# Kernel optimization log

Measured on AMD Instinct MI355X. Metric: run time of the kernel, lower is better.

The kernel has to match this reference:

```python
import jax, jax.numpy as jnp
import numpy as np
import math

D_MODEL = 1024
N_HEADS = 16
HEAD_DIM = D_MODEL // N_HEADS  # 64
R = HEAD_DIM // 2              # 32
ROPE_BASE = 10000.0
B, T = 4, 2048


def setup_inputs() -> dict:
    key = jax.random.key(0)
    k1, k2, k3, k4, k5 = jax.random.split(key, 5)
    x = jax.random.normal(k1, (B, T, D_MODEL), dtype=jnp.float32)
    Wqkv = jax.random.normal(k2, (3 * D_MODEL, D_MODEL), dtype=jnp.float32) * (1.0 / math.sqrt(D_MODEL))
    Wout = jax.random.normal(k3, (D_MODEL, D_MODEL), dtype=jnp.float32) * (1.0 / math.sqrt(D_MODEL))
    alpha = jax.random.normal(k4, (N_HEADS, R), dtype=jnp.float32) * 0.01
    beta = jax.random.normal(k5, (N_HEADS, R), dtype=jnp.float32) * 0.01
    return {"x": x, "Wqkv": Wqkv, "Wout": Wout, "alpha": alpha, "beta": beta}


def _fourier_bias(alpha, beta, t):
    # omega[r] = base^{-2r/head_dim}, same geometric spacing as RoPE
    omega = ROPE_BASE ** (-2.0 * jnp.arange(R, dtype=jnp.float32) / HEAD_DIM)
    # bias depends only on displacement i-j in [-(t-1), t-1]: compute once per
    # displacement, then gather into the (t, t) matrix (same math as full T x T).
    disp = jnp.arange(-(t - 1), t, dtype=jnp.float32)            # (2t-1,)
    angles = omega[:, None] * disp[None, :]                       # (R, 2t-1)
    vec = jnp.einsum('hr,rk->hk', alpha, jnp.cos(angles)) \
        + jnp.einsum('hr,rk->hk', beta, jnp.sin(angles))          # (H, 2t-1)
    i = jnp.arange(t)
    idx = i[:, None] - i[None, :] + (t - 1)                       # (t, t), delta[i,j]=i-j
    return vec[:, idx]                                            # (H, t, t)


def reference(x, Wqkv, Wout, alpha, beta):
    b, t, d = x.shape
    qkv = x @ Wqkv.T                                              # (B, T, 3D)
    q, k, v = jnp.split(qkv, 3, axis=-1)
    def heads(a):
        return a.reshape(b, t, N_HEADS, HEAD_DIM).transpose(0, 2, 1, 3)  # (B,H,T,dh)
    q, k, v = heads(q), heads(k), heads(v)
    scale = 1.0 / math.sqrt(HEAD_DIM)
    logits = jnp.einsum('bhqd,bhkd->bhqk', q, k) * scale          # (B,H,T,T)
    logits = logits + _fourier_bias(alpha, beta, t)[None]
    causal = jnp.tril(jnp.ones((t, t), dtype=bool))
    logits = jnp.where(causal[None, None], logits, -jnp.inf)
    attn = jax.nn.softmax(logits, axis=-1)
    out = jnp.einsum('bhqk,bhkd->bhqd', attn, v)                  # (B,H,T,dh)
    out = out.transpose(0, 2, 1, 3).reshape(b, t, d)
    return out @ Wout.T
```

## Files before the change

kernel.cpp:

```cpp
#include <hip/hip_runtime.h>
#include <cstdint>
#include <cstddef>

typedef _Float16 f16;
typedef f16 f16x8 __attribute__((ext_vector_type(8)));
typedef __fp16 fp16x2 __attribute__((ext_vector_type(2)));
typedef float f32x4 __attribute__((ext_vector_type(4)));
typedef float f32x16 __attribute__((ext_vector_type(16)));
typedef uint32_t u32;


__device__ __forceinline__ void gload16(const void* g, void* l) {
  __builtin_amdgcn_global_load_lds((const __attribute__((address_space(1))) void*)g,
                                   (__attribute__((address_space(3))) void*)l,
                                   16u, 0, 0u);
}

__device__ __forceinline__ u32 pkrtz(float a, float b) {
  union { fp16x2 v; u32 u; } t;
  t.v = __builtin_amdgcn_cvt_pkrtz(a, b);
  return t.u;
}

__device__ __forceinline__ u32 packh2(float a, float b) { return pkrtz(a, b); }

__device__ __forceinline__ float max3f(float a, float b, float c) {
  return fmaxf(fmaxf(a, b), c);
}

__device__ __forceinline__ void pl32swap(u32& a, u32& b) {
  asm volatile("v_permlane32_swap_b32 %0, %1" : "+v"(a), "+v"(b));
}


__global__ __launch_bounds__(256) void cvt_f32_f16(const float* __restrict__ in,
                                                   f16* __restrict__ out, int n) {
  int i = (blockIdx.x * 256 + threadIdx.x) * 8;
  if (i >= n) return;
  float4 a = *(const float4*)(in + i);
  float4 b = *(const float4*)(in + i + 4);
  f16x8 o;
  o[0] = (f16)a.x; o[1] = (f16)a.y; o[2] = (f16)a.z; o[3] = (f16)a.w;
  o[4] = (f16)b.x; o[5] = (f16)b.y; o[6] = (f16)b.z; o[7] = (f16)b.w;
  *(f16x8*)(out + i) = o;
}


__global__ __launch_bounds__(256) void build_tables(const float* __restrict__ alpha,
                                                    const float* __restrict__ beta,
                                                    f16* __restrict__ U,
                                                    f16* __restrict__ Wt) {
  int idx = blockIdx.x * 256 + threadIdx.x;
  int t = idx >> 5, r = idx & 31;
  float w = powf(10000.0f, -(float)r / 32.0f);
  float ang = w * (float)t;
  float c = cosf(ang), s = sinf(ang);
  const float L2E = 1.44269504089f;
  U[t * 64 + 2 * r]     = (f16)(c * L2E);
  U[t * 64 + 2 * r + 1] = (f16)(s * L2E);
  #pragma unroll
  for (int h = 0; h < 16; ++h) {
    float al = alpha[h * 32 + r], be = beta[h * 32 + r];
    Wt[(size_t)(h * 2048 + t) * 64 + 2 * r]     = (f16)(al * c - be * s);
    Wt[(size_t)(h * 2048 + t) * 64 + 2 * r + 1] = (f16)(al * s + be * c);
  }
}


__global__ __launch_bounds__(256) void gemm_qkv(const f16* __restrict__ A,
                                                const f16* __restrict__ B,
                                                f16* __restrict__ Q,
                                                f16* __restrict__ Kh,
                                                f16* __restrict__ Vt) {
  __shared__ __align__(16) char sm[65536];
  const int K = 1024;
  int tid = threadIdx.x;
  int lane = tid & 63, wid = tid >> 6;
  int bid = blockIdx.x;
  int xcd = bid & 7;
  int id = bid >> 3;
  int nl = id / 64;
  int m0 = (id & 63) * 128;
  int n0 = (xcd * 3 + nl) * 128;
  int wm = wid >> 1, wn = wid & 1;
  int c = lane & 15, g = lane >> 4, l7 = lane & 7;

  int srow[4], sce[4], sdst[4];
  #pragma unroll
  for (int i = 0; i < 4; ++i) {
    int p = i * 4096 + tid * 16;
    int q = p ^ (((p >> 7) & 7) << 4);
    srow[i] = q >> 7; sce[i] = (q & 127) >> 1;
    sdst[i] = i * 4096 + wid * 1024;
  }

  f32x4 acc[4][4] = {};

  #pragma unroll
  for (int i = 0; i < 4; ++i) {
    gload16(A + (size_t)(m0 + srow[i]) * K + sce[i], sm + sdst[i]);
    gload16(B + (size_t)(n0 + srow[i]) * K + sce[i], sm + 32768 + sdst[i]);
  }

  for (int kt = 0; kt < 16; ++kt) {
    int cur = kt & 1;
    char* As = sm + cur * 16384;
    char* Bs = sm + 32768 + cur * 16384;

    if (kt < 15) {
      char* Ad = sm + (cur ^ 1) * 16384;
      char* Bd = sm + 32768 + (cur ^ 1) * 16384;
      #pragma unroll
      for (int i = 0; i < 4; ++i) {
        gload16(A + (size_t)(m0 + srow[i]) * K + (kt + 1) * 64 + sce[i], Ad + sdst[i]);
        gload16(B + (size_t)(n0 + srow[i]) * K + (kt + 1) * 64 + sce[i], Bd + sdst[i]);
      }
      asm volatile("s_waitcnt vmcnt(8)" ::: "memory");
    } else {
      asm volatile("s_waitcnt vmcnt(0)" ::: "memory");
    }
    __builtin_amdgcn_s_barrier();

    __builtin_amdgcn_s_setprio(1);
    #pragma unroll
    for (int kk = 0; kk < 2; ++kk) {
      int co = (kk * 64 + g * 16) ^ (l7 << 4);
      f16x8 af[4], bf[4];
      #pragma unroll
      for (int fr = 0; fr < 4; ++fr)
        af[fr] = *(const f16x8*)(As + (wm * 64 + fr * 16 + c) * 128 + co);
      #pragma unroll
      for (int fn = 0; fn < 4; ++fn)
        bf[fn] = *(const f16x8*)(Bs + (wn * 64 + fn * 16 + c) * 128 + co);
      #pragma unroll
      for (int fr = 0; fr < 4; ++fr)
        #pragma unroll
        for (int fn = 0; fn < 4; ++fn)
          acc[fr][fn] = __builtin_amdgcn_mfma_f32_16x16x32_f16(af[fr], bf[fn], acc[fr][fn], 0, 0, 0);
    }
    __builtin_amdgcn_s_setprio(0);
    __builtin_amdgcn_s_barrier();
  }

  int which = n0 >> 10;
  #pragma unroll
  for (int fr = 0; fr < 4; ++fr) {
    int m = m0 + wm * 64 + fr * 16 + g * 4;
    int b = m >> 11, t = m & 2047;
    #pragma unroll
    for (int fn = 0; fn < 4; ++fn) {
      int n = n0 + wn * 64 + fn * 16 + c;
      int nf = n & 1023, hh = nf >> 6, d = nf & 63;
      if (which == 0) {
        #pragma unroll
        for (int r = 0; r < 4; ++r)
          Q[(size_t)((b * 16 + hh) * 2048 + (t + r)) * 64 + d] = (f16)(acc[fr][fn][r] * 0.180336880111f);
      } else if (which == 1) {
        #pragma unroll
        for (int r = 0; r < 4; ++r)
          Kh[(size_t)((b * 16 + hh) * 2048 + (t + r)) * 64 + d] = (f16)acc[fr][fn][r];
      } else {
        uint2 pk;
        pk.x = packh2(acc[fr][fn][0], acc[fr][fn][1]);
        pk.y = packh2(acc[fr][fn][2], acc[fr][fn][3]);
        *(uint2*)(Vt + (size_t)((b * 16 + hh) * 64 + d) * 2048 + t) = pk;
      }
    }
  }
}


__global__ __launch_bounds__(256) void gemm_out(const f16* __restrict__ A,
                                                const f16* __restrict__ B,
                                                float* __restrict__ Cout) {
  __shared__ __align__(16) char sm[65536];
  const int K = 1024;
  int tid = threadIdx.x;
  int lane = tid & 63, wid = tid >> 6;
  int bid = blockIdx.x;
  int xcd = bid & 7;
  int id = bid >> 3;
  int m0 = id * 128;
  int n0 = xcd * 128;
  int wm = wid >> 1, wn = wid & 1;
  int c = lane & 15, g = lane >> 4, l7 = lane & 7;

  int srow[4], sce[4], sdst[4];
  #pragma unroll
  for (int i = 0; i < 4; ++i) {
    int p = i * 4096 + tid * 16;
    int q = p ^ (((p >> 7) & 7) << 4);
    srow[i] = q >> 7; sce[i] = (q & 127) >> 1;
    sdst[i] = i * 4096 + wid * 1024;
  }

  f32x4 acc[4][4] = {};

  #pragma unroll
  for (int i = 0; i < 4; ++i) {
    gload16(A + (size_t)(m0 + srow[i]) * K + sce[i], sm + sdst[i]);
    gload16(B + (size_t)(n0 + srow[i]) * K + sce[i], sm + 32768 + sdst[i]);
  }

  for (int kt = 0; kt < 16; ++kt) {
    int cur = kt & 1;
    char* As = sm + cur * 16384;
    char* Bs = sm + 32768 + cur * 16384;

    if (kt < 15) {
      char* Ad = sm + (cur ^ 1) * 16384;
      char* Bd = sm + 32768 + (cur ^ 1) * 16384;
      #pragma unroll
      for (int i = 0; i < 4; ++i) {
        gload16(A + (size_t)(m0 + srow[i]) * K + (kt + 1) * 64 + sce[i], Ad + sdst[i]);
        gload16(B + (size_t)(n0 + srow[i]) * K + (kt + 1) * 64 + sce[i], Bd + sdst[i]);
      }
      asm volatile("s_waitcnt vmcnt(8)" ::: "memory");
    } else {
      asm volatile("s_waitcnt vmcnt(0)" ::: "memory");
    }
    __builtin_amdgcn_s_barrier();

    __builtin_amdgcn_s_setprio(1);
    #pragma unroll
    for (int kk = 0; kk < 2; ++kk) {
      int co = (kk * 64 + g * 16) ^ (l7 << 4);
      f16x8 af[4], bf[4];
      #pragma unroll
      for (int fr = 0; fr < 4; ++fr)
        af[fr] = *(const f16x8*)(As + (wm * 64 + fr * 16 + c) * 128 + co);
      #pragma unroll
      for (int fn = 0; fn < 4; ++fn)
        bf[fn] = *(const f16x8*)(Bs + (wn * 64 + fn * 16 + c) * 128 + co);
      #pragma unroll
      for (int fr = 0; fr < 4; ++fr)
        #pragma unroll
        for (int fn = 0; fn < 4; ++fn)
          acc[fr][fn] = __builtin_amdgcn_mfma_f32_16x16x32_f16(af[fr], bf[fn], acc[fr][fn], 0, 0, 0);
    }
    __builtin_amdgcn_s_setprio(0);
    __builtin_amdgcn_s_barrier();
  }

  #pragma unroll
  for (int fr = 0; fr < 4; ++fr) {
    int m = m0 + wm * 64 + fr * 16 + g * 4;
    #pragma unroll
    for (int fn = 0; fn < 4; ++fn) {
      int n = n0 + wn * 64 + fn * 16 + c;
      #pragma unroll
      for (int r = 0; r < 4; ++r)
        Cout[(size_t)(m + r) * 1024 + n] = acc[fr][fn][r];
    }
  }
}


__global__ __launch_bounds__(512, 2) void attn(const f16* __restrict__ Q,
                                               const f16* __restrict__ Kh,
                                               const f16* __restrict__ Vt,
                                               const f16* __restrict__ U,
                                               const f16* __restrict__ Wt,
                                               f16* __restrict__ AO) {
  __shared__ __align__(16) char sm[98304];
  int tid = threadIdx.x, lane = tid & 63, wid = tid >> 6;
  int l31 = lane & 31, hi = lane >> 5;
  int o = blockIdx.x;
  int pr = o >> 6;
  int bh = o & 63;
  int h = bh & 15, b = bh >> 4;
  int swz = (lane & 15) << 4;

  const f16* ksrc[4]; int kdst[4];
  #pragma unroll
  for (int i = 0; i < 4; ++i) {
    int p = i * 8192 + tid * 16;
    int row = p >> 8;
    int col = (p & 255) ^ ((row & 15) << 4);
    int ce = col >> 1;
    ksrc[i] = (ce < 64) ? (Kh + (size_t)(bh * 2048 + row) * 64 + ce)
                        : (Wt + (size_t)(h * 2048 + row) * 64 + (ce - 64));
    kdst[i] = i * 8192 + wid * 1024;
  }
  const f16* vsrc[2]; int vdst[2];
  #pragma unroll
  for (int i = 0; i < 2; ++i) {
    int p = i * 8192 + tid * 16;
    int row = p >> 8;
    int col = (p & 255) ^ ((row & 15) << 4);
    int ce = col >> 1;
    vsrc[i] = Vt + (size_t)(bh * 64 + row) * 2048 + ce;
    vdst[i] = i * 8192 + wid * 1024;
  }

  #pragma unroll 1
  for (int pass = 0; pass < 2; ++pass) {
    int qt = pass ? pr : 7 - pr;
    int qrow = qt * 256 + wid * 32 + l31;
    int ktmax = 2 * qt + 1;

    f16x8 qf[8];
    {
      const f16* qp = Q + (size_t)(bh * 2048 + qrow) * 64 + hi * 8;
      const f16* up = U + (size_t)qrow * 64 + hi * 8;
      #pragma unroll
      for (int ks = 0; ks < 4; ++ks) {
        qf[ks]     = *(const f16x8*)(qp + ks * 16);
        qf[4 + ks] = *(const f16x8*)(up + ks * 16);
      }
    }

    float m_i = -1e30f, l_i = 0.0f;
    f32x16 accA = {}, accB = {};

    #pragma unroll
    for (int i = 0; i < 4; ++i) gload16(ksrc[i], sm + kdst[i]);
    #pragma unroll
    for (int i = 0; i < 2; ++i) gload16(vsrc[i], sm + 65536 + vdst[i]);
    __syncthreads();

    for (int kt = 0; kt <= ktmax; ++kt) {
      int cur = kt & 1;
      char* Ks = sm + cur * 32768;
      char* Vs = sm + 65536 + cur * 16384;

      if (kt < ktmax) {
        char* kb = sm + (cur ^ 1) * 32768;
        char* vb = sm + 65536 + (cur ^ 1) * 16384;
        #pragma unroll
        for (int i = 0; i < 4; ++i) gload16(ksrc[i] + (size_t)(kt + 1) * 8192, kb + kdst[i]);
        #pragma unroll
        for (int i = 0; i < 2; ++i) gload16(vsrc[i] + (size_t)(kt + 1) * 128, vb + vdst[i]);
      }

      f32x16 st0 = {}, st1 = {}, st2 = {}, st3 = {};
      __builtin_amdgcn_s_setprio(1);
      #pragma unroll
      for (int ks = 0; ks < 8; ++ks) {
        int co = (ks * 32 + hi * 16) ^ swz;
        f16x8 k0 = *(const f16x8*)(Ks + l31 * 256 + co);
        f16x8 k1 = *(const f16x8*)(Ks + (32 + l31) * 256 + co);
        f16x8 k2 = *(const f16x8*)(Ks + (64 + l31) * 256 + co);
        f16x8 k3 = *(const f16x8*)(Ks + (96 + l31) * 256 + co);
        st0 = __builtin_amdgcn_mfma_f32_32x32x16_f16(k0, qf[ks], st0, 0, 0, 0);
        st1 = __builtin_amdgcn_mfma_f32_32x32x16_f16(k1, qf[ks], st1, 0, 0, 0);
        st2 = __builtin_amdgcn_mfma_f32_32x32x16_f16(k2, qf[ks], st2, 0, 0, 0);
        st3 = __builtin_amdgcn_mfma_f32_32x32x16_f16(k3, qf[ks], st3, 0, 0, 0);
      }
      __builtin_amdgcn_s_setprio(0);

      int kv0 = kt * 128;
      if (kv0 + 127 > qt * 256 + wid * 32) {
        #pragma unroll
        for (int r = 0; r < 16; ++r) {
          int kvl = kv0 + (r & 3) + 8 * (r >> 2) + 4 * hi;
          if (kvl > qrow) st0[r] = -1e30f;
          if (kvl + 32 > qrow) st1[r] = -1e30f;
          if (kvl + 64 > qrow) st2[r] = -1e30f;
          if (kvl + 96 > qrow) st3[r] = -1e30f;
        }
      }

      float pm = fmaxf(fmaxf(st0[0], st1[0]), fmaxf(st2[0], st3[0]));
      #pragma unroll
      for (int r = 1; r < 16; ++r) {
        pm = max3f(pm, st0[r], st1[r]);
        pm = max3f(pm, st2[r], st3[r]);
      }
      pm = fmaxf(pm, __shfl_xor(pm, 32, 64));
      if (!__all(pm <= m_i + 8.0f)) {
        float mnew = fmaxf(m_i, pm);
        float sc = __builtin_amdgcn_exp2f(m_i - mnew);
        l_i *= sc;
        accA *= sc;
        accB *= sc;
        m_i = mnew;
      }

      float ps = 0.0f;
      u32 pk0[8], pk1[8], pk2[8], pk3[8];
      #pragma unroll
      for (int j = 0; j < 8; ++j) {
        float a0 = __builtin_amdgcn_exp2f(st0[2 * j] - m_i);
        float a1 = __builtin_amdgcn_exp2f(st0[2 * j + 1] - m_i);
        float b0 = __builtin_amdgcn_exp2f(st1[2 * j] - m_i);
        float b1 = __builtin_amdgcn_exp2f(st1[2 * j + 1] - m_i);
        float c0 = __builtin_amdgcn_exp2f(st2[2 * j] - m_i);
        float c1 = __builtin_amdgcn_exp2f(st2[2 * j + 1] - m_i);
        float d0 = __builtin_amdgcn_exp2f(st3[2 * j] - m_i);
        float d1 = __builtin_amdgcn_exp2f(st3[2 * j + 1] - m_i);
        ps += (a0 + a1) + (b0 + b1) + (c0 + c1) + (d0 + d1);
        pk0[j] = pkrtz(a0, a1);
        pk1[j] = pkrtz(b0, b1);
        pk2[j] = pkrtz(c0, c1);
        pk3[j] = pkrtz(d0, d1);
      }
      ps += __shfl_xor(ps, 32, 64);
      l_i += ps;

      pl32swap(pk0[0], pk0[2]); pl32swap(pk0[1], pk0[3]);
      pl32swap(pk0[4], pk0[6]); pl32swap(pk0[5], pk0[7]);
      pl32swap(pk1[0], pk1[2]); pl32swap(pk1[1], pk1[3]);
      pl32swap(pk1[4], pk1[6]); pl32swap(pk1[5], pk1[7]);
      pl32swap(pk2[0], pk2[2]); pl32swap(pk2[1], pk2[3]);
      pl32swap(pk2[4], pk2[6]); pl32swap(pk2[5], pk2[7]);
      pl32swap(pk3[0], pk3[2]); pl32swap(pk3[1], pk3[3]);
      pl32swap(pk3[4], pk3[6]); pl32swap(pk3[5], pk3[7]);

      __builtin_amdgcn_s_setprio(1);
      #pragma unroll
      for (int kb = 0; kb < 8; ++kb) {
        union { u32 w[4]; f16x8 v; } bf;
        const u32* pk = (kb < 2) ? pk0 : (kb < 4) ? pk1 : (kb < 6) ? pk2 : pk3;
        int base = (kb & 1) * 4;
        bf.w[0] = pk[base + 0]; bf.w[1] = pk[base + 1];
        bf.w[2] = pk[base + 2]; bf.w[3] = pk[base + 3];
        int co = (kb * 32 + hi * 16) ^ swz;
        f16x8 v0 = *(const f16x8*)(Vs + l31 * 256 + co);
        f16x8 v1 = *(const f16x8*)(Vs + (32 + l31) * 256 + co);
        accA = __builtin_amdgcn_mfma_f32_32x32x16_f16(v0, bf.v, accA, 0, 0, 0);
        accB = __builtin_amdgcn_mfma_f32_32x32x16_f16(v1, bf.v, accB, 0, 0, 0);
      }
      __builtin_amdgcn_s_setprio(0);
      __syncthreads();
    }

    float inv = __builtin_amdgcn_rcpf(l_i);
    f16* aop = AO + (size_t)(b * 2048 + qrow) * 1024 + h * 64;
    #pragma unroll
    for (int u = 0; u < 4; ++u) {
      uint2 ov;
      ov.x = pkrtz(accA[4 * u] * inv, accA[4 * u + 1] * inv);
      ov.y = pkrtz(accA[4 * u + 2] * inv, accA[4 * u + 3] * inv);
      *(uint2*)(aop + 8 * u + 4 * hi) = ov;
      ov.x = pkrtz(accB[4 * u] * inv, accB[4 * u + 1] * inv);
      ov.y = pkrtz(accB[4 * u + 2] * inv, accB[4 * u + 3] * inv);
      *(uint2*)(aop + 32 + 8 * u + 4 * hi) = ov;
    }
  }
}


extern "C" void kernel_launch(void* const* d_in, const int* in_sizes, int n_in,
                              void* d_out, int out_size, void* d_ws, size_t ws_size,
                              hipStream_t stream) {
  const float* x     = (const float*)d_in[0];
  const float* Wqkv  = (const float*)d_in[1];
  const float* Wout  = (const float*)d_in[2];
  const float* alpha = (const float*)d_in[3];
  const float* beta  = (const float*)d_in[4];

  char* ws = (char*)d_ws;
  f16* Xh    = (f16*)(ws);
  f16* Wqkvh = (f16*)(ws + 16777216);
  f16* Wouth = (f16*)(ws + 23068672);
  f16* Qh    = (f16*)(ws + 25165824);
  f16* Kh    = (f16*)(ws + 41943040);
  f16* Vt    = (f16*)(ws + 58720256);
  f16* U     = (f16*)(ws + 75497472);
  f16* Wt    = (f16*)(ws + 75759616);
  f16* AO    = Xh;

  cvt_f32_f16<<<4096, 256, 0, stream>>>(x, Xh, 8388608);
  cvt_f32_f16<<<1536, 256, 0, stream>>>(Wqkv, Wqkvh, 3145728);
  cvt_f32_f16<<<512, 256, 0, stream>>>(Wout, Wouth, 1048576);
  build_tables<<<256, 256, 0, stream>>>(alpha, beta, U, Wt);
  gemm_qkv<<<1536, 256, 0, stream>>>(Xh, Wqkvh, Qh, Kh, Vt);
  attn<<<256, 512, 0, stream>>>(Qh, Kh, Vt, U, Wt, AO);
  gemm_out<<<512, 256, 0, stream>>>(AO, Wouth, (float*)d_out);
}
```

Measured before the change: 186.4 us.

## Software-pipeline QK^T of next tile with softmax and PV of current tile

Restructures the attention loop so the QK^T MFMAs for the next KV tile are issued before the softmax and PV work of the current tile. K tiles are now prefetched two iterations ahead and V one ahead, with a prologue that loads two K tiles and computes the first scores. The aim is to hide exp/max latency behind matrix-core work, at the cost of another 64 accumulator registers per lane, which may lower occupancy or cause spills.

```diff
diff --git a/kernel.cpp b/kernel.cpp
--- a/kernel.cpp
+++ b/kernel.cpp
@@ -317,23 +317,13 @@
     for (int i = 0; i < 4; ++i) gload16(ksrc[i], sm + kdst[i]);
     #pragma unroll
     for (int i = 0; i < 2; ++i) gload16(vsrc[i], sm + 65536 + vdst[i]);
+    #pragma unroll
+    for (int i = 0; i < 4; ++i) gload16(ksrc[i] + 8192, sm + 32768 + kdst[i]);
     __syncthreads();
 
-    for (int kt = 0; kt <= ktmax; ++kt) {
-      int cur = kt & 1;
-      char* Ks = sm + cur * 32768;
-      char* Vs = sm + 65536 + cur * 16384;
-
-      if (kt < ktmax) {
-        char* kb = sm + (cur ^ 1) * 32768;
-        char* vb = sm + 65536 + (cur ^ 1) * 16384;
-        #pragma unroll
-        for (int i = 0; i < 4; ++i) gload16(ksrc[i] + (size_t)(kt + 1) * 8192, kb + kdst[i]);
-        #pragma unroll
-        for (int i = 0; i < 2; ++i) gload16(vsrc[i] + (size_t)(kt + 1) * 128, vb + vdst[i]);
-      }
-
-      f32x16 st0 = {}, st1 = {}, st2 = {}, st3 = {};
+    f32x16 stC0 = {}, stC1 = {}, stC2 = {}, stC3 = {};
+    {
+      char* Ks = sm;
       __builtin_amdgcn_s_setprio(1);
       #pragma unroll
       for (int ks = 0; ks < 8; ++ks) {
@@ -342,30 +332,64 @@
         f16x8 k1 = *(const f16x8*)(Ks + (32 + l31) * 256 + co);
         f16x8 k2 = *(const f16x8*)(Ks + (64 + l31) * 256 + co);
         f16x8 k3 = *(const f16x8*)(Ks + (96 + l31) * 256 + co);
-        st0 = __builtin_amdgcn_mfma_f32_32x32x16_f16(k0, qf[ks], st0, 0, 0, 0);
-        st1 = __builtin_amdgcn_mfma_f32_32x32x16_f16(k1, qf[ks], st1, 0, 0, 0);
-        st2 = __builtin_amdgcn_mfma_f32_32x32x16_f16(k2, qf[ks], st2, 0, 0, 0);
-        st3 = __builtin_amdgcn_mfma_f32_32x32x16_f16(k3, qf[ks], st3, 0, 0, 0);
+        stC0 = __builtin_amdgcn_mfma_f32_32x32x16_f16(k0, qf[ks], stC0, 0, 0, 0);
+        stC1 = __builtin_amdgcn_mfma_f32_32x32x16_f16(k1, qf[ks], stC1, 0, 0, 0);
+        stC2 = __builtin_amdgcn_mfma_f32_32x32x16_f16(k2, qf[ks], stC2, 0, 0, 0);
+        stC3 = __builtin_amdgcn_mfma_f32_32x32x16_f16(k3, qf[ks], stC3, 0, 0, 0);
       }
       __builtin_amdgcn_s_setprio(0);
+    }
+
+    for (int kt = 0; kt <= ktmax; ++kt) {
+      char* Vs = sm + 65536 + (kt & 1) * 16384;
+
+      if (kt + 1 <= ktmax) {
+        char* vb = sm + 65536 + ((kt + 1) & 1) * 16384;
+        #pragma unroll
+        for (int i = 0; i < 2; ++i) gload16(vsrc[i] + (size_t)(kt + 1) * 128, vb + vdst[i]);
+      }
+      if (kt + 2 <= ktmax) {
+        char* kb = sm + (kt & 1) * 32768;
+        #pragma unroll
+        for (int i = 0; i < 4; ++i) gload16(ksrc[i] + (size_t)(kt + 2) * 8192, kb + kdst[i]);
+      }
+
+      f32x16 stN0 = {}, stN1 = {}, stN2 = {}, stN3 = {};
+      if (kt < ktmax) {
+        char* Ks = sm + ((kt + 1) & 1) * 32768;
+        __builtin_amdgcn_s_setprio(1);
+        #pragma unroll
+        for (int ks = 0; ks < 8; ++ks) {
+          int co = (ks * 32 + hi * 16) ^ swz;
+          f16x8 k0 = *(const f16x8*)(Ks + l31 * 256 + co);
+          f16x8 k1 = *(const f16x8*)(Ks + (32 + l31) * 256 + co);
+          f16x8 k2 = *(const f16x8*)(Ks + (64 + l31) * 256 + co);
+          f16x8 k3 = *(const f16x8*)(Ks + (96 + l31) * 256 + co);
+          stN0 = __builtin_amdgcn_mfma_f32_32x32x16_f16(k0, qf[ks], stN0, 0, 0, 0);
+          stN1 = __builtin_amdgcn_mfma_f32_32x32x16_f16(k1, qf[ks], stN1, 0, 0, 0);
+          stN2 = __builtin_amdgcn_mfma_f32_32x32x16_f16(k2, qf[ks], stN2, 0, 0, 0);
+          stN3 = __builtin_amdgcn_mfma_f32_32x32x16_f16(k3, qf[ks], stN3, 0, 0, 0);
+        }
+        __builtin_amdgcn_s_setprio(0);
+      }
 
       int kv0 = kt * 128;
       if (kv0 + 127 > qt * 256 + wid * 32) {
         #pragma unroll
         for (int r = 0; r < 16; ++r) {
           int kvl = kv0 + (r & 3) + 8 * (r >> 2) + 4 * hi;
-          if (kvl > qrow) st0[r] = -1e30f;
-          if (kvl + 32 > qrow) st1[r] = -1e30f;
-          if (kvl + 64 > qrow) st2[r] = -1e30f;
-          if (kvl + 96 > qrow) st3[r] = -1e30f;
+          if (kvl > qrow) stC0[r] = -1e30f;
+          if (kvl + 32 > qrow) stC1[r] = -1e30f;
+          if (kvl + 64 > qrow) stC2[r] = -1e30f;
+          if (kvl + 96 > qrow) stC3[r] = -1e30f;
         }
       }
 
-      float pm = fmaxf(fmaxf(st0[0], st1[0]), fmaxf(st2[0], st3[0]));
+      float pm = fmaxf(fmaxf(stC0[0], stC1[0]), fmaxf(stC2[0], stC3[0]));
       #pragma unroll
       for (int r = 1; r < 16; ++r) {
-        pm = max3f(pm, st0[r], st1[r]);
-        pm = max3f(pm, st2[r], st3[r]);
+        pm = max3f(pm, stC0[r], stC1[r]);
+        pm = max3f(pm, stC2[r], stC3[r]);
       }
       pm = fmaxf(pm, __shfl_xor(pm, 32, 64));
       if (!__all(pm <= m_i + 8.0f)) {
@@ -381,14 +405,14 @@
       u32 pk0[8], pk1[8], pk2[8], pk3[8];
       #pragma unroll
       for (int j = 0; j < 8; ++j) {
-        float a0 = __builtin_amdgcn_exp2f(st0[2 * j] - m_i);
-        float a1 = __builtin_amdgcn_exp2f(st0[2 * j + 1] - m_i);
-        float b0 = __builtin_amdgcn_exp2f(st1[2 * j] - m_i);
-        float b1 = __builtin_amdgcn_exp2f(st1[2 * j + 1] - m_i);
-        float c0 = __builtin_amdgcn_exp2f(st2[2 * j] - m_i);
-        float c1 = __builtin_amdgcn_exp2f(st2[2 * j + 1] - m_i);
-        float d0 = __builtin_amdgcn_exp2f(st3[2 * j] - m_i);
-        float d1 = __builtin_amdgcn_exp2f(st3[2 * j + 1] - m_i);
+        float a0 = __builtin_amdgcn_exp2f(stC0[2 * j] - m_i);
+        float a1 = __builtin_amdgcn_exp2f(stC0[2 * j + 1] - m_i);
+        float b0 = __builtin_amdgcn_exp2f(stC1[2 * j] - m_i);
+        float b1 = __builtin_amdgcn_exp2f(stC1[2 * j + 1] - m_i);
+        float c0 = __builtin_amdgcn_exp2f(stC2[2 * j] - m_i);
+        float c1 = __builtin_amdgcn_exp2f(stC2[2 * j + 1] - m_i);
+        float d0 = __builtin_amdgcn_exp2f(stC3[2 * j] - m_i);
+        float d1 = __builtin_amdgcn_exp2f(stC3[2 * j + 1] - m_i);
         ps += (a0 + a1) + (b0 + b1) + (c0 + c1) + (d0 + d1);
         pk0[j] = pkrtz(a0, a1);
         pk1[j] = pkrtz(b0, b1);
@@ -423,6 +447,8 @@
       }
       __builtin_amdgcn_s_setprio(0);
       __syncthreads();
+
+      stC0 = stN0; stC1 = stN1; stC2 = stN2; stC3 = stN3;
     }
 
     float inv = __builtin_amdgcn_rcpf(l_i);
```

Result: slower. 193.3 us (+3.7%).
